# Performance work log

Hardware: AMD Instinct MI355X
Metric: run time of the kernel (lower is better)

The kernel has to match this reference:

```python
import jax, jax.numpy as jnp
import numpy as np

N_NODES = 100000
N_EMBED = 64
N_HIDDEN = 64
N_EDGES = 1200000


def setup_inputs() -> dict:
    key = jax.random.key(0)
    ks = jax.random.split(key, 8)
    prop_edge_index = jax.random.randint(ks[0], (2, N_EDGES), 0, N_NODES, dtype=jnp.int64)
    emb = jax.random.normal(ks[1], (N_NODES, N_EMBED), dtype=jnp.float32) * 0.05
    # ChebConv K=2 -> two linear weights per layer + bias
    W1_0 = jax.random.normal(ks[2], (N_EMBED, N_HIDDEN), dtype=jnp.float32) * 0.05
    W1_1 = jax.random.normal(ks[3], (N_EMBED, N_HIDDEN), dtype=jnp.float32) * 0.05
    b1 = jnp.zeros((N_HIDDEN,), dtype=jnp.float32)
    W2_0 = jax.random.normal(ks[4], (N_HIDDEN, N_HIDDEN), dtype=jnp.float32) * 0.05
    W2_1 = jax.random.normal(ks[5], (N_HIDDEN, N_HIDDEN), dtype=jnp.float32) * 0.05
    b2 = jnp.zeros((N_HIDDEN,), dtype=jnp.float32)
    return {"prop_edge_index": prop_edge_index, "emb": emb,
            "W1_0": W1_0, "W1_1": W1_1, "b1": b1,
            "W2_0": W2_0, "W2_1": W2_1, "b2": b2}


def _cheb_norm(edge_index, num_nodes):
    """PyG ChebConv.__norm__ with sym normalization, lambda_max=2.0.
    L_hat = 2L/lambda_max - I = (I - D^-1/2 A D^-1/2) - I, so the net
    diagonal weight is 0 and off-diagonal weight is -d_i^-1/2 * d_j^-1/2.
    Self loops in the input are removed first (weight 0)."""
    row, col = edge_index[0], edge_index[1]
    w = jnp.where(row != col, 1.0, 0.0).astype(jnp.float32)  # remove_self_loops
    deg = jax.ops.segment_sum(w, row, num_segments=num_nodes)
    dinv = jnp.where(deg > 0, deg ** -0.5, 0.0)
    norm = -dinv[row] * w * dinv[col]
    return norm


def _cheb_conv(x, src, dst, norm, W0, W1, b, num_nodes):
    # K=2: out = T0(x) @ W0 + T1(x) @ W1 + b, T0 = x, T1 = L_hat x
    Tx1 = jax.ops.segment_sum(norm[:, None] * x[src], dst, num_segments=num_nodes)
    return x @ W0 + Tx1 @ W1 + b


def reference(prop_edge_index, emb, W1_0, W1_1, b1, W2_0, W2_1, b2):
    src, dst = prop_edge_index[0], prop_edge_index[1]
    norm = _cheb_norm(prop_edge_index, N_NODES)
    x = _cheb_conv(emb, src, dst, norm, W1_0, W1_1, b1, N_NODES)
    x = jax.nn.relu(x)
    # dropout: eval mode (identity)
    x = _cheb_conv(x, src, dst, norm, W2_0, W2_1, b2, N_NODES)
    return x
```

## Files before the change

### kernel.cpp

```cpp
#include <hip/hip_runtime.h>

#define N_NODES 100000
#define N_EDGES 1200000
#define NF 64

typedef __attribute__((ext_vector_type(8))) short short8;
typedef __attribute__((ext_vector_type(4))) float float4v;

__device__ __forceinline__ ushort f2bf(float f) {
    unsigned u = __float_as_uint(f);
    return (ushort)((u + 0x7FFF + ((u >> 16) & 1)) >> 16);
}

#define NBINS 196
#define CAP 7680
#define EPB 2560
#define NBLK 469

#define OFF_CNT    0
#define OFF_ENDP   400128
#define OFF_DINV   800256
#define OFF_CUR    1200384
#define OFF_PKW    1202048
#define OFF_SRCS   1234816
#define OFF_SBIN   7255936
#define OFF_DBIN   10266496
#define OFF_EMBBF  16287616
#define OFF_HBF    29087616

__global__ __launch_bounds__(256) void prepsort(const float* __restrict__ W10,
                                                const float* __restrict__ W11,
                                                const float* __restrict__ W20,
                                                const float* __restrict__ W21,
                                                ushort* __restrict__ pk,
                                                const float* __restrict__ emb,
                                                ushort* __restrict__ emb_bf,
                                                const int* __restrict__ row,
                                                const int* __restrict__ col,
                                                int* __restrict__ cur,
                                                ushort* __restrict__ sbinned,
                                                int* __restrict__ dbinned) {
    int b = blockIdx.x;
    int t = threadIdx.x;
    if (b < NBLK) {
        __shared__ int2 ecache[EPB];
        __shared__ int sh[NBINS], dh[NBINS];
        __shared__ int sbase[NBINS], dbase[NBINS];
        if (t < NBINS) { sh[t] = 0; dh[t] = 0; }
        __syncthreads();
        int base = b * EPB;
        for (int k = 0; k < EPB / 256; ++k) {
            int e = base + k * 256 + t;
            int s = -1, d = -1;
            if (e < N_EDGES) { s = row[e]; d = col[e]; }
            ecache[k * 256 + t] = make_int2(s, d);
            if (s >= 0 && s != d) {
                atomicAdd(&sh[s >> 9], 1);
                atomicAdd(&dh[d >> 9], 1);
            }
        }
        __syncthreads();
        if (t < NBINS) {
            sbase[t] = t * CAP + atomicAdd(&cur[t], sh[t]);
            dbase[t] = t * CAP + atomicAdd(&cur[NBINS + t], dh[t]);
        }
        __syncthreads();
        for (int k = 0; k < EPB / 256; ++k) {
            int2 p = ecache[k * 256 + t];
            int s = p.x, d = p.y;
            if (s >= 0 && s != d) {
                int ss = atomicAdd(&sbase[s >> 9], 1);
                sbinned[ss] = (ushort)(s & 511);
                int ds = atomicAdd(&dbase[d >> 9], 1);
                dbinned[ds] = (s << 9) | (d & 511);
            }
        }
    } else if (b < NBLK + 8) {
        int idx = (b - NBLK) * 256 + t;
        int layer = idx >> 10;
        int rest = idx & 1023;
        int f = rest >> 6, L = rest & 63;
        int n = (f & 3) * 16 + (L & 15);
        int kb = (f >> 2) * 32 + ((L >> 4) << 3);
#pragma unroll
        for (int j = 0; j < 8; ++j) {
            int k = kb + j;
            const float* W = layer ? ((k < 64) ? W20 : W21) : ((k < 64) ? W10 : W11);
            pk[idx * 8 + j] = f2bf(W[(k & 63) * 64 + n]);
        }
    } else {
        int bb = b - NBLK - 8;
        int i = (bb * 256 + t) * 8;
        float4 v0 = *(const float4*)(emb + i);
        float4 v1 = *(const float4*)(emb + i + 4);
        uint4 o;
        o.x = (uint)f2bf(v0.x) | ((uint)f2bf(v0.y) << 16);
        o.y = (uint)f2bf(v0.z) | ((uint)f2bf(v0.w) << 16);
        o.z = (uint)f2bf(v1.x) | ((uint)f2bf(v1.y) << 16);
        o.w = (uint)f2bf(v1.z) | ((uint)f2bf(v1.w) << 16);
        *(uint4*)(emb_bf + i) = o;
    }
}

__global__ __launch_bounds__(512) void build(const ushort* __restrict__ sbinned,
                                             const int* __restrict__ dbinned,
                                             const int* __restrict__ cur,
                                             float* __restrict__ dinv,
                                             int* __restrict__ cnt,
                                             int* __restrict__ endp,
                                             int* __restrict__ srcs) {
    int t = threadIdx.x;
    int b = blockIdx.x;
    if (b < NBINS) {
        __shared__ int hist[512];
        hist[t] = 0;
        __syncthreads();
        int start = b * CAP;
        int end = start + cur[b];
        for (int i = start + t; i < end; i += 512)
            atomicAdd(&hist[sbinned[i]], 1);
        __syncthreads();
        int n0 = (b << 9) + t;
        if (n0 < N_NODES) dinv[n0] = hist[t] ? rsqrtf((float)hist[t]) : 0.0f;
    } else {
        int bb = b - NBINS;
        __shared__ int ecache[CAP];
        __shared__ int hist[512];
        __shared__ int lcur[512];
        __shared__ int tot_s;
        hist[t] = 0;
        __syncthreads();
        int start = bb * CAP;
        int len = cur[NBINS + bb];
        for (int i = t; i < len; i += 512) {
            int p = dbinned[start + i];
            ecache[i] = p;
            atomicAdd(&hist[p & 511], 1);
        }
        __syncthreads();
        int o0 = hist[t];
        int A0 = (o0 + 3) & ~3;
        __syncthreads();
        hist[t] = A0;
        __syncthreads();
        for (int off = 1; off < 512; off <<= 1) {
            int v = (t >= off) ? hist[t - off] : 0;
            __syncthreads();
            hist[t] += v;
            __syncthreads();
        }
        int e0 = hist[t] - A0;
        if (t == 511) tot_s = hist[511];
        lcur[t] = start + e0;
        int n0 = (bb << 9) + t;
        if (n0 < N_NODES) { cnt[n0] = o0; endp[n0] = start + e0 + o0; }
        __syncthreads();
        for (int i = t; i < len; i += 512) {
            int p = ecache[i];
            int slot = atomicAdd(&lcur[p & 511], 1);
            srcs[slot] = p >> 9;
        }
        __syncthreads();
        for (int k = o0; k < A0; ++k) srcs[start + e0 + k] = 0;
        if (t < 16) srcs[start + tot_s + t] = 0;
    }
}

#define NPW 16
#define WPB 2
#define NPB (NPW * WPB)
#define LB2 ((N_NODES + NPB - 1) / NPB)

__global__ __launch_bounds__(128, 8) void cheb_layer(const ushort* __restrict__ x,
                                                     const int* __restrict__ srcs,
                                                     const float* __restrict__ dinv,
                                                     const int* __restrict__ endp,
                                                     const int* __restrict__ cnt,
                                                     const ushort* __restrict__ pk,
                                                     const float* __restrict__ bias,
                                                     ushort* __restrict__ out_bf,
                                                     float* __restrict__ out_f32,
                                                     int last) {
    __shared__ ushort sA[WPB][16][136];

    int t = threadIdx.x;
    int lane = t & 63, wid = t >> 6;
    int c = lane & 15, q = lane >> 4;
    int qd = q, fg = c;
    int nb = blockIdx.x * NPB + wid * NPW;

    int nend = 0, ncnt = 0;
    if (lane < NPW && nb + lane < N_NODES) {
        nend = endp[nb + lane];
        ncnt = cnt[nb + lane];
    }

    const uint2* xr = (const uint2*)x;

    auto chunk8 = [&](int eb, int eendL, float& a0, float& a1, float& a2, float& a3) {
        int4 sv = *(const int4*)(srcs + eb);
        int4 sw = *(const int4*)(srcs + eb + 4);
        int sA01 = (qd & 1) ? sv.y : sv.x;
        int sA23 = (qd & 1) ? sv.w : sv.z;
        int srcA = (qd & 2) ? sA23 : sA01;
        int sB01 = (qd & 1) ? sw.y : sw.x;
        int sB23 = (qd & 1) ? sw.w : sw.z;
        int srcB = (qd & 2) ? sB23 : sB01;
        float nAf = dinv[srcA];
        float nBf = dinv[srcB];
        nAf = (eb + qd < eendL) ? nAf : 0.0f;
        nBf = (eb + 4 + qd < eendL) ? nBf : 0.0f;
        uint2 gA = xr[(size_t)srcA * 16 + fg];
        uint2 gB = xr[(size_t)srcB * 16 + fg];
        a0 = fmaf(nAf, __uint_as_float(gA.x << 16), a0);
        a1 = fmaf(nAf, __uint_as_float(gA.x & 0xffff0000u), a1);
        a2 = fmaf(nAf, __uint_as_float(gA.y << 16), a2);
        a3 = fmaf(nAf, __uint_as_float(gA.y & 0xffff0000u), a3);
        a0 = fmaf(nBf, __uint_as_float(gB.x << 16), a0);
        a1 = fmaf(nBf, __uint_as_float(gB.x & 0xffff0000u), a1);
        a2 = fmaf(nBf, __uint_as_float(gB.y << 16), a2);
        a3 = fmaf(nBf, __uint_as_float(gB.y & 0xffff0000u), a3);
    };

#pragma unroll
    for (int gp = 0; gp < NPW; gp += 2) {
        int cn0 = __builtin_amdgcn_readlane(ncnt, gp);
        int ee0 = __builtin_amdgcn_readlane(nend, gp);
        int cn1 = __builtin_amdgcn_readlane(ncnt, gp + 1);
        int ee1 = __builtin_amdgcn_readlane(nend, gp + 1);
        int s0 = ee0 - cn0, s1 = ee1 - cn1;
        float a0 = 0, a1 = 0, a2 = 0, a3 = 0;
        float b0 = 0, b1 = 0, b2 = 0, b3 = 0;

        chunk8(s0,     ee0, a0, a1, a2, a3);
        chunk8(s1,     ee1, b0, b1, b2, b3);
        chunk8(s0 + 8, ee0, a0, a1, a2, a3);
        chunk8(s1 + 8, ee1, b0, b1, b2, b3);
        for (int e = s0 + 16; e < ee0; e += 8) chunk8(e, ee0, a0, a1, a2, a3);
        for (int e = s1 + 16; e < ee1; e += 8) chunk8(e, ee1, b0, b1, b2, b3);

        a0 += __shfl_xor(a0, 16, 64); b0 += __shfl_xor(b0, 16, 64);
        a1 += __shfl_xor(a1, 16, 64); b1 += __shfl_xor(b1, 16, 64);
        a2 += __shfl_xor(a2, 16, 64); b2 += __shfl_xor(b2, 16, 64);
        a3 += __shfl_xor(a3, 16, 64); b3 += __shfl_xor(b3, 16, 64);
        a0 += __shfl_xor(a0, 32, 64); b0 += __shfl_xor(b0, 32, 64);
        a1 += __shfl_xor(a1, 32, 64); b1 += __shfl_xor(b1, 32, 64);
        a2 += __shfl_xor(a2, 32, 64); b2 += __shfl_xor(b2, 32, 64);
        a3 += __shfl_xor(a3, 32, 64); b3 += __shfl_xor(b3, 32, 64);

        int node0 = nb + gp, node1 = nb + gp + 1;
        int ni0 = (node0 < N_NODES) ? node0 : 0;
        int ni1 = (node1 < N_NODES) ? node1 : 0;
        if (qd == 0) {
            uint2 xv0 = xr[(size_t)ni0 * 16 + fg];
            uint2 xv1 = xr[(size_t)ni1 * 16 + fg];
            *(uint2*)&sA[wid][gp][4 * fg] = xv0;
            *(uint2*)&sA[wid][gp + 1][4 * fg] = xv1;
        }
        if (qd == 1) {
            float sc0 = -dinv[ni0];
            float sc1 = -dinv[ni1];
            uint2 p0, p1;
            p0.x = (uint)f2bf(a0 * sc0) | ((uint)f2bf(a1 * sc0) << 16);
            p0.y = (uint)f2bf(a2 * sc0) | ((uint)f2bf(a3 * sc0) << 16);
            p1.x = (uint)f2bf(b0 * sc1) | ((uint)f2bf(b1 * sc1) << 16);
            p1.y = (uint)f2bf(b2 * sc1) | ((uint)f2bf(b3 * sc1) << 16);
            *(uint2*)&sA[wid][gp][64 + 4 * fg] = p0;
            *(uint2*)&sA[wid][gp + 1][64 + 4 * fg] = p1;
        }
    }
    __builtin_amdgcn_wave_barrier();

    const short8* pk8 = (const short8*)pk;
    float4v C[4];
#pragma unroll
    for (int nt = 0; nt < 4; ++nt) {
        float b = bias[nt * 16 + c];
        C[nt] = (float4v){b, b, b, b};
    }
#pragma unroll
    for (int kt = 0; kt < 4; ++kt) {
        short8 af = *(const short8*)&sA[wid][c][kt * 32 + q * 8];
#pragma unroll
        for (int nt = 0; nt < 4; ++nt) {
            short8 bfr = pk8[(kt * 4 + nt) * 64 + lane];
            C[nt] = __builtin_amdgcn_mfma_f32_16x16x32_bf16(af, bfr, C[nt], 0, 0, 0);
        }
    }

#pragma unroll
    for (int nt = 0; nt < 4; ++nt) {
#pragma unroll
        for (int i = 0; i < 4; ++i) {
            int node = nb + q * 4 + i;
            if (node < N_NODES) {
                float v = C[nt][i];
                if (!last) {
                    v = fmaxf(v, 0.0f);
                    out_bf[(size_t)node * NF + nt * 16 + c] = f2bf(v);
                } else {
                    out_f32[(size_t)node * NF + nt * 16 + c] = v;
                }
            }
        }
    }
}

extern "C" void kernel_launch(void* const* d_in, const int* in_sizes, int n_in,
                              void* d_out, int out_size, void* d_ws, size_t ws_size,
                              hipStream_t stream) {
    const int* ei = (const int*)d_in[0];
    const int* row = ei;
    const int* col = ei + N_EDGES;
    const float* emb = (const float*)d_in[1];
    const float* W1_0 = (const float*)d_in[2];
    const float* W1_1 = (const float*)d_in[3];
    const float* b1 = (const float*)d_in[4];
    const float* W2_0 = (const float*)d_in[5];
    const float* W2_1 = (const float*)d_in[6];
    const float* b2 = (const float*)d_in[7];
    float* out = (float*)d_out;

    char* ws = (char*)d_ws;
    int* cnt = (int*)(ws + OFF_CNT);
    int* endp = (int*)(ws + OFF_ENDP);
    float* dinv = (float*)(ws + OFF_DINV);
    int* cur = (int*)(ws + OFF_CUR);
    ushort* pk = (ushort*)(ws + OFF_PKW);
    int* srcs = (int*)(ws + OFF_SRCS);
    ushort* sbinned = (ushort*)(ws + OFF_SBIN);
    int* dbinned = (int*)(ws + OFF_DBIN);
    ushort* emb_bf = (ushort*)(ws + OFF_EMBBF);
    ushort* h_bf = (ushort*)(ws + OFF_HBF);

    hipMemsetAsync(cur, 0, 2 * NBINS * sizeof(int), stream);
    prepsort<<<NBLK + 8 + 3125, 256, 0, stream>>>(W1_0, W1_1, W2_0, W2_1, pk,
                                                  emb, emb_bf, row, col, cur,
                                                  sbinned, dbinned);
    build<<<2 * NBINS, 512, 0, stream>>>(sbinned, dbinned, cur, dinv, cnt, endp, srcs);

    cheb_layer<<<LB2, 128, 0, stream>>>(emb_bf, srcs, dinv, endp, cnt, pk, b1, h_bf, nullptr, 0);
    cheb_layer<<<LB2, 128, 0, stream>>>(h_bf, srcs, dinv, endp, cnt, pk + 8192, b2, nullptr, out, 1);
}
```

Baseline: 203.4 us.

## Stage binned edges in shared memory for coalesced scatter in prep and build

The binning kernel now handles twice as many edges per block with 512 threads. It runs a local prefix scan over bin counts and sorts each block's edges by bin in shared memory, then writes them out contiguously per bin instead of scattering individual global writes. The CSR build kernel likewise assembles its per-bin srcs output in a shared buffer and copies it out linearly, reading the binned input twice instead of caching it. This is meant to make global stores coalesced, at the cost of more shared memory per block, extra barriers and a second read of row/col and dbinned.

```diff
diff --git a/kernel.cpp b/kernel.cpp
--- a/kernel.cpp
+++ b/kernel.cpp
@@ -14,8 +14,8 @@
 
 #define NBINS 196
 #define CAP 7680
-#define EPB 2560
-#define NBLK 469
+#define EPB 5120
+#define NBLK 235
 
 #define OFF_CNT    0
 #define OFF_ENDP   400128
@@ -28,7 +28,7 @@
 #define OFF_EMBBF  16287616
 #define OFF_HBF    29087616
 
-__global__ __launch_bounds__(256) void prepsort(const float* __restrict__ W10,
+__global__ __launch_bounds__(512) void prepsort(const float* __restrict__ W10,
                                                 const float* __restrict__ W11,
                                                 const float* __restrict__ W20,
                                                 const float* __restrict__ W21,
@@ -43,40 +43,70 @@
     int b = blockIdx.x;
     int t = threadIdx.x;
     if (b < NBLK) {
-        __shared__ int2 ecache[EPB];
         __shared__ int sh[NBINS], dh[NBINS];
-        __shared__ int sbase[NBINS], dbase[NBINS];
-        if (t < NBINS) { sh[t] = 0; dh[t] = 0; }
+        __shared__ int sst[NBINS], dstt[NBINS];
+        __shared__ int sgb[NBINS], dgb[NBINS];
+        __shared__ int slc[NBINS], dlc[NBINS];
+        __shared__ int ssc[256], dsc[256];
+        __shared__ ushort sloc[EPB];
+        __shared__ int dloc[EPB];
+        __shared__ unsigned char sbid[EPB], dbid[EPB];
+        for (int i = t; i < NBINS; i += 512) { sh[i] = 0; dh[i] = 0; }
         __syncthreads();
         int base = b * EPB;
-        for (int k = 0; k < EPB / 256; ++k) {
-            int e = base + k * 256 + t;
-            int s = -1, d = -1;
-            if (e < N_EDGES) { s = row[e]; d = col[e]; }
-            ecache[k * 256 + t] = make_int2(s, d);
-            if (s >= 0 && s != d) {
-                atomicAdd(&sh[s >> 9], 1);
-                atomicAdd(&dh[d >> 9], 1);
+        for (int k = 0; k < EPB / 512; ++k) {
+            int e = base + k * 512 + t;
+            if (e < N_EDGES) {
+                int s = row[e], d = col[e];
+                if (s != d) { atomicAdd(&sh[s >> 9], 1); atomicAdd(&dh[d >> 9], 1); }
             }
         }
         __syncthreads();
+        int cs = 0, cd = 0;
         if (t < NBINS) {
-            sbase[t] = t * CAP + atomicAdd(&cur[t], sh[t]);
-            dbase[t] = t * CAP + atomicAdd(&cur[NBINS + t], dh[t]);
-        }
-        __syncthreads();
-        for (int k = 0; k < EPB / 256; ++k) {
-            int2 p = ecache[k * 256 + t];
-            int s = p.x, d = p.y;
-            if (s >= 0 && s != d) {
-                int ss = atomicAdd(&sbase[s >> 9], 1);
-                sbinned[ss] = (ushort)(s & 511);
-                int ds = atomicAdd(&dbase[d >> 9], 1);
-                dbinned[ds] = (s << 9) | (d & 511);
+            cs = sh[t]; cd = dh[t];
+            sgb[t] = t * CAP + atomicAdd(&cur[t], cs);
+            dgb[t] = t * CAP + atomicAdd(&cur[NBINS + t], cd);
+        }
+        if (t < 256) { ssc[t] = (t < NBINS) ? cs : 0; dsc[t] = (t < NBINS) ? cd : 0; }
+        __syncthreads();
+        for (int off = 1; off < 256; off <<= 1) {
+            int vs = 0, vd = 0;
+            if (t < 256 && t >= off) { vs = ssc[t - off]; vd = dsc[t - off]; }
+            __syncthreads();
+            if (t < 256 && t >= off) { ssc[t] += vs; dsc[t] += vd; }
+            __syncthreads();
+        }
+        if (t < NBINS) {
+            sst[t] = ssc[t] - cs; slc[t] = sst[t];
+            dstt[t] = dsc[t] - cd; dlc[t] = dstt[t];
+        }
+        __syncthreads();
+        for (int k = 0; k < EPB / 512; ++k) {
+            int e = base + k * 512 + t;
+            if (e < N_EDGES) {
+                int s = row[e], d = col[e];
+                if (s != d) {
+                    int sb = s >> 9, db = d >> 9;
+                    int ls = atomicAdd(&slc[sb], 1);
+                    sloc[ls] = (ushort)(s & 511); sbid[ls] = (unsigned char)sb;
+                    int ld = atomicAdd(&dlc[db], 1);
+                    dloc[ld] = (s << 9) | (d & 511); dbid[ld] = (unsigned char)db;
+                }
             }
         }
-    } else if (b < NBLK + 8) {
-        int idx = (b - NBLK) * 256 + t;
+        __syncthreads();
+        int totS = ssc[255], totD = dsc[255];
+        for (int i = t; i < totS; i += 512) {
+            int bi = sbid[i];
+            sbinned[sgb[bi] + (i - sst[bi])] = sloc[i];
+        }
+        for (int i = t; i < totD; i += 512) {
+            int bi = dbid[i];
+            dbinned[dgb[bi] + (i - dstt[bi])] = dloc[i];
+        }
+    } else if (b < NBLK + 4) {
+        int idx = (b - NBLK) * 512 + t;
         int layer = idx >> 10;
         int rest = idx & 1023;
         int f = rest >> 6, L = rest & 63;
@@ -89,16 +119,18 @@
             pk[idx * 8 + j] = f2bf(W[(k & 63) * 64 + n]);
         }
     } else {
-        int bb = b - NBLK - 8;
-        int i = (bb * 256 + t) * 8;
-        float4 v0 = *(const float4*)(emb + i);
-        float4 v1 = *(const float4*)(emb + i + 4);
-        uint4 o;
-        o.x = (uint)f2bf(v0.x) | ((uint)f2bf(v0.y) << 16);
-        o.y = (uint)f2bf(v0.z) | ((uint)f2bf(v0.w) << 16);
-        o.z = (uint)f2bf(v1.x) | ((uint)f2bf(v1.y) << 16);
-        o.w = (uint)f2bf(v1.z) | ((uint)f2bf(v1.w) << 16);
-        *(uint4*)(emb_bf + i) = o;
+        int bb = b - NBLK - 4;
+        int i = (bb * 512 + t) * 8;
+        if (i < N_NODES * NF) {
+            float4 v0 = *(const float4*)(emb + i);
+            float4 v1 = *(const float4*)(emb + i + 4);
+            uint4 o;
+            o.x = (uint)f2bf(v0.x) | ((uint)f2bf(v0.y) << 16);
+            o.y = (uint)f2bf(v0.z) | ((uint)f2bf(v0.w) << 16);
+            o.z = (uint)f2bf(v1.x) | ((uint)f2bf(v1.y) << 16);
+            o.w = (uint)f2bf(v1.z) | ((uint)f2bf(v1.w) << 16);
+            *(uint4*)(emb_bf + i) = o;
+        }
     }
 }
 
@@ -116,27 +148,24 @@
         hist[t] = 0;
         __syncthreads();
         int start = b * CAP;
-        int end = start + cur[b];
-        for (int i = start + t; i < end; i += 512)
-            atomicAdd(&hist[sbinned[i]], 1);
+        int len = cur[b];
+        for (int i = t; i < len; i += 512)
+            atomicAdd(&hist[sbinned[start + i]], 1);
         __syncthreads();
         int n0 = (b << 9) + t;
         if (n0 < N_NODES) dinv[n0] = hist[t] ? rsqrtf((float)hist[t]) : 0.0f;
     } else {
         int bb = b - NBINS;
-        __shared__ int ecache[CAP];
         __shared__ int hist[512];
         __shared__ int lcur[512];
+        __shared__ int obuf[CAP];
         __shared__ int tot_s;
         hist[t] = 0;
         __syncthreads();
         int start = bb * CAP;
         int len = cur[NBINS + bb];
-        for (int i = t; i < len; i += 512) {
-            int p = dbinned[start + i];
-            ecache[i] = p;
-            atomicAdd(&hist[p & 511], 1);
-        }
+        for (int i = t; i < len; i += 512)
+            atomicAdd(&hist[dbinned[start + i] & 511], 1);
         __syncthreads();
         int o0 = hist[t];
         int A0 = (o0 + 3) & ~3;
@@ -151,18 +180,21 @@
         }
         int e0 = hist[t] - A0;
         if (t == 511) tot_s = hist[511];
-        lcur[t] = start + e0;
+        lcur[t] = e0;
         int n0 = (bb << 9) + t;
         if (n0 < N_NODES) { cnt[n0] = o0; endp[n0] = start + e0 + o0; }
         __syncthreads();
         for (int i = t; i < len; i += 512) {
-            int p = ecache[i];
+            int p = dbinned[start + i];
             int slot = atomicAdd(&lcur[p & 511], 1);
-            srcs[slot] = p >> 9;
-        }
-        __syncthreads();
-        for (int k = o0; k < A0; ++k) srcs[start + e0 + k] = 0;
-        if (t < 16) srcs[start + tot_s + t] = 0;
+            obuf[slot] = p >> 9;
+        }
+        for (int k = o0; k < A0; ++k) obuf[e0 + k] = 0;
+        __syncthreads();
+        if (t < 16) obuf[tot_s + t] = 0;
+        __syncthreads();
+        int tot = tot_s + 16;
+        for (int i = t; i < tot; i += 512) srcs[start + i] = obuf[i];
     }
 }
 
@@ -334,7 +366,7 @@
     ushort* h_bf = (ushort*)(ws + OFF_HBF);
 
     hipMemsetAsync(cur, 0, 2 * NBINS * sizeof(int), stream);
-    prepsort<<<NBLK + 8 + 3125, 256, 0, stream>>>(W1_0, W1_1, W2_0, W2_1, pk,
+    prepsort<<<NBLK + 4 + 1563, 512, 0, stream>>>(W1_0, W1_1, W2_0, W2_1, pk,
                                                   emb, emb_bf, row, col, cur,
                                                   sbinned, dbinned);
     build<<<2 * NBINS, 512, 0, stream>>>(sbinned, dbinned, cur, dinv, cnt, endp, srcs);
```

Measured after the change: 188.9 us. -7.1%, faster.
